# Optimization experiments

Measured on AMD Instinct MI355X. Metric: run time of the kernel, lower is better.

The kernel has to match this reference:

```python
import jax, jax.numpy as jnp
import numpy as np

TOPK = 2
ALPHA = 32.0
EPS = 1e-20


def setup_inputs() -> dict:
    key = jax.random.key(0)
    ks = jax.random.split(key, 6)
    E, D, R, Q, V = 16, 2048, 16, 2048, 512
    B, S = 2, 2048
    return {
        "hidden_states": jax.random.normal(ks[0], (B, S, D), jnp.float32),
        "router_weight": jax.random.normal(ks[1], (E, D), jnp.float32) * 0.02,
        "q_lora_a": jax.random.normal(ks[2], (E, D, R), jnp.float32) * 0.02,
        "q_lora_b": jax.random.normal(ks[3], (E, R, Q), jnp.float32) * 0.02,
        "v_lora_a": jax.random.normal(ks[4], (E, D, R), jnp.float32) * 0.02,
        "v_lora_b": jax.random.normal(ks[5], (E, R, V), jnp.float32) * 0.02,
    }


def reference(hidden_states, router_weight, q_lora_a, q_lora_b, v_lora_a, v_lora_b):
    E, D, R = q_lora_a.shape
    Qo = q_lora_b.shape[-1]
    Vo = v_lora_b.shape[-1]
    scale = ALPHA / float(R)
    orig_shape = hidden_states.shape[:-1]
    h = hidden_states.reshape(-1, D)  # [n, D]
    n = h.shape[0]

    # router: top-k softmax probs, renormalized over the k selected experts
    logits = jnp.einsum('nd,ed->ne', h, router_weight)
    probs = jax.nn.softmax(logits, axis=-1)
    scores, idx = jax.lax.top_k(probs, TOPK)          # [n, k]
    scores = scores / (scores.sum(-1, keepdims=True) + EPS)

    # per-token expert combine weights c[n, e] = scale * sum_k score_k * 1[idx_k == e]
    c = jnp.zeros((n, E), h.dtype).at[jnp.arange(n)[:, None], idx].add(scores * scale)

    # dense per-expert low-rank projections; weighting by c makes non-selected
    # experts contribute zero -> identical math to gather + einsum + weighted sum.
    q_low = jnp.einsum('nd,edr->ner', h, q_lora_a) * c[..., None]  # [n, E, R]
    v_low = jnp.einsum('nd,edr->ner', h, v_lora_a) * c[..., None]
    q_delta = jnp.einsum('ner,erq->nq', q_low, q_lora_b)
    v_delta = jnp.einsum('ner,erv->nv', v_low, v_lora_b)

    return (q_delta.reshape(*orig_shape, Qo), v_delta.reshape(*orig_shape, Vo))
```

## Files before the change

kernel.cpp:

```cpp
#include <hip/hip_runtime.h>
#include <math.h>

#define DD 2048
#define EE 16
#define RR 16
#define QO 2048
#define VO 512
#define TILE 128
#define BATCH 16
#define DSPLIT 4
#define DRANGE (DD / DSPLIT)
#define DC 64
#define HSTR (DC + 4)
#define ASTR 20
#define RDC 256
#define T2 32
#define CGQ (QO / 256)
#define CGV (VO / 256)

struct Route { int i0, i1; float w0, w1; };

__global__ __launch_bounds__(256) void router_kernel(
    const float* __restrict__ h, const float* __restrict__ rw,
    Route* __restrict__ route, int n)
{
    __shared__ float  hs[8 * RDC];
    __shared__ double slogd[8 * EE];

    int t0 = blockIdx.x * 8;
    int e  = threadIdx.x >> 4;
    int l  = threadIdx.x & 15;

    double acc[8];
#pragma unroll
    for (int t = 0; t < 8; ++t) acc[t] = 0.0;

    for (int d0 = 0; d0 < DD; d0 += RDC) {
        __syncthreads();
        for (int i = threadIdx.x; i < 8 * (RDC / 4); i += 256) {
            int t = i >> 6, dq = (i & 63) * 4;
            float4 v = make_float4(0.f, 0.f, 0.f, 0.f);
            if (t0 + t < n)
                v = *(const float4*)&h[(size_t)(t0 + t) * DD + d0 + dq];
            *(float4*)&hs[t * RDC + dq] = v;
        }
        __syncthreads();
        const float* rwe = rw + e * DD + d0;
#pragma unroll
        for (int g = 0; g < RDC / 64; ++g) {
            int d = g * 64 + l * 4;
            float4 r4 = *(const float4*)&rwe[d];
            double rx = r4.x, ry = r4.y, rz = r4.z, rw4 = r4.w;
#pragma unroll
            for (int t = 0; t < 8; ++t) {
                float4 hv = *(const float4*)&hs[t * RDC + d];
                acc[t] += (double)hv.x * rx + (double)hv.y * ry
                        + (double)hv.z * rz + (double)hv.w * rw4;
            }
        }
    }
#pragma unroll
    for (int t = 0; t < 8; ++t) {
#pragma unroll
        for (int off = 8; off; off >>= 1)
            acc[t] += __shfl_down(acc[t], off, 16);
    }
    if (l == 0) {
#pragma unroll
        for (int t = 0; t < 8; ++t) slogd[t * EE + e] = acc[t];
    }
    __syncthreads();

    if (threadIdx.x < 8) {
        int t = threadIdx.x, tok = t0 + t;
        if (tok < n) {
            double lg[EE];
#pragma unroll
            for (int i = 0; i < EE; ++i) lg[i] = slogd[t * EE + i];
            int i0 = 0;
            for (int i = 1; i < EE; ++i) if (lg[i] > lg[i0]) i0 = i;
            int i1 = -1;
            for (int i = 0; i < EE; ++i)
                if (i != i0 && (i1 < 0 || lg[i] > lg[i1])) i1 = i;
            double mx = lg[i0], Z = 0.0;
            for (int i = 0; i < EE; ++i) Z += exp(lg[i] - mx);
            double p0 = 1.0 / Z;
            double p1 = exp(lg[i1] - mx) / Z;
            double s  = p0 + p1 + 1e-20;
            Route rt;
            rt.i0 = i0; rt.i1 = i1;
            rt.w0 = (float)(2.0 * p0 / s);
            rt.w1 = (float)(2.0 * p1 / s);
            route[tok] = rt;
        }
    }
}

__global__ __launch_bounds__(256) void a_kernel(
    const float* __restrict__ h, const Route* __restrict__ route,
    const float* __restrict__ qa, const float* __restrict__ va,
    float* __restrict__ low, int n)
{
    int e  = blockIdx.x;
    int t0 = blockIdx.y * TILE;
    int ds = blockIdx.z;

    __shared__ int   sel_tok[TILE];
    __shared__ float sel_w[TILE];
    __shared__ int   sel_k[TILE];
    __shared__ int   sm_cnt;
    if (threadIdx.x == 0) sm_cnt = 0;
    __syncthreads();
    for (int i = threadIdx.x; i < TILE; i += 256) {
        int tok = t0 + i;
        if (tok < n) {
            Route rt = route[tok];
            float w = 0.f; int sel = 0, k = 0;
            if      (rt.i0 == e) { sel = 1; w = rt.w0; k = 0; }
            else if (rt.i1 == e) { sel = 1; w = rt.w1; k = 1; }
            if (sel) {
                int p = atomicAdd(&sm_cnt, 1);
                sel_tok[p] = tok; sel_w[p] = w; sel_k[p] = k;
            }
        }
    }
    __syncthreads();
    int m = sm_cnt;
    if (m == 0) return;

    __align__(16) __shared__ float aq_s[DC * ASTR];
    __align__(16) __shared__ float av_s[DC * ASTR];
    __align__(16) __shared__ float hs[BATCH * HSTR];

    const float* qa_e = qa + (size_t)e * DD * RR;
    const float* va_e = va + (size_t)e * DD * RR;

    int s    = threadIdx.x & 15;
    int tile = threadIdx.x >> 4;
    int tp   = tile >> 2;
    int rp   = tile & 3;

    for (int b0 = 0; b0 < m; b0 += BATCH) {
        int mb = min(BATCH, m - b0);

        float accq[4][4], accv[4][4];
#pragma unroll
        for (int ti = 0; ti < 4; ++ti)
#pragma unroll
            for (int ri = 0; ri < 4; ++ri) { accq[ti][ri] = 0.f; accv[ti][ri] = 0.f; }

        for (int d0 = ds * DRANGE; d0 < (ds + 1) * DRANGE; d0 += DC) {
            __syncthreads();
            {
                int i = threadIdx.x;
                int d = i >> 2, rf = (i & 3) * 4;
                *(float4*)&aq_s[d * ASTR + rf] = *(const float4*)&qa_e[(size_t)(d0 + d) * RR + rf];
                *(float4*)&av_s[d * ASTR + rf] = *(const float4*)&va_e[(size_t)(d0 + d) * RR + rf];
            }
            {
                int i = threadIdx.x;
                int j = i >> 4, dq = (i & 15) * 4;
                float4 v = make_float4(0.f, 0.f, 0.f, 0.f);
                if (j < mb)
                    v = *(const float4*)&h[(size_t)sel_tok[b0 + j] * DD + d0 + dq];
                *(float4*)&hs[j * HSTR + dq] = v;
            }
            __syncthreads();
#pragma unroll
            for (int dd = 0; dd < DC / 16; ++dd) {
                int d = (dd << 4) + s;
                float hv[4];
#pragma unroll
                for (int ti = 0; ti < 4; ++ti)
                    hv[ti] = hs[(tp * 4 + ti) * HSTR + d];
                float4 aqv = *(const float4*)&aq_s[d * ASTR + rp * 4];
                float4 avv = *(const float4*)&av_s[d * ASTR + rp * 4];
                const float* aqp = &aqv.x;
                const float* avp = &avv.x;
#pragma unroll
                for (int ti = 0; ti < 4; ++ti)
#pragma unroll
                    for (int ri = 0; ri < 4; ++ri) {
                        accq[ti][ri] = fmaf(hv[ti], aqp[ri], accq[ti][ri]);
                        accv[ti][ri] = fmaf(hv[ti], avp[ri], accv[ti][ri]);
                    }
            }
        }
#pragma unroll
        for (int ti = 0; ti < 4; ++ti)
#pragma unroll
            for (int ri = 0; ri < 4; ++ri) {
#pragma unroll
                for (int off = 8; off; off >>= 1) {
                    accq[ti][ri] += __shfl_down(accq[ti][ri], off, 16);
                    accv[ti][ri] += __shfl_down(accv[ti][ri], off, 16);
                }
            }
        if (s == 0) {
#pragma unroll
            for (int ti = 0; ti < 4; ++ti) {
                int t = tp * 4 + ti;
                if (t < mb) {
                    int   tok = sel_tok[b0 + t];
                    int   k   = sel_k[b0 + t];
                    float w   = sel_w[b0 + t];
                    size_t base = ((size_t)(tok * 2 + k) * DSPLIT + ds) * 32;
#pragma unroll
                    for (int ri = 0; ri < 4; ++ri) {
                        low[base + rp * 4 + ri]      = accq[ti][ri] * w;
                        low[base + 16 + rp * 4 + ri] = accv[ti][ri] * w;
                    }
                }
            }
        }
        __syncthreads();
    }
}

__global__ __launch_bounds__(256) void b_kernel(
    const Route* __restrict__ route, const float* __restrict__ low,
    const float* __restrict__ qb, const float* __restrict__ vb,
    float* __restrict__ outq, float* __restrict__ outv, int n)
{
    int t0 = blockIdx.x * T2;
    int cg = blockIdx.y;
    int tid = threadIdx.x;

    __shared__ float acc_s[T2 * 256];
    __shared__ float ls[T2 * 2 * RR];
    __shared__ int   elist[EE * T2];
    __shared__ int   ecnt[EE];
    __shared__ Route rts[T2];

    if (tid < EE) ecnt[tid] = 0;
    if (tid < T2) {
        int tok = t0 + tid;
        if (tok < n) rts[tid] = route[tok];
        else { rts[tid].i0 = -1; rts[tid].i1 = -1; rts[tid].w0 = 0.f; rts[tid].w1 = 0.f; }
    }
    __syncthreads();
    if (tid < T2 * 2) {
        int j = tid >> 1, k = tid & 1;
        int e = k ? rts[j].i1 : rts[j].i0;
        if (e >= 0) {
            int p = atomicAdd(&ecnt[e], 1);
            elist[e * T2 + p] = j * 2 + k;
        }
    }
    int side = (cg >= CGQ) ? 1 : 0;
    {
        int slot = tid >> 2, r4 = (tid & 3) * 4;
        int j = slot >> 1, k = slot & 1;
        int tok = t0 + j;
        float4 v = make_float4(0.f, 0.f, 0.f, 0.f);
        if (tok < n) {
            const float* lp = low + (size_t)(tok * 2 + k) * (DSPLIT * 32) + side * 16 + r4;
            float4 p0 = *(const float4*)(lp);
            float4 p1 = *(const float4*)(lp + 32);
            float4 p2 = *(const float4*)(lp + 64);
            float4 p3 = *(const float4*)(lp + 96);
            v.x = p0.x + p1.x + p2.x + p3.x;
            v.y = p0.y + p1.y + p2.y + p3.y;
            v.z = p0.z + p1.z + p2.z + p3.z;
            v.w = p0.w + p1.w + p2.w + p3.w;
        }
        *(float4*)&ls[slot * RR + r4] = v;
    }
#pragma unroll
    for (int j = 0; j < T2; ++j) acc_s[j * 256 + tid] = 0.f;
    __syncthreads();

    const float* bp; float* outp; int W, colbase;
    if (cg < CGQ) { bp = qb; outp = outq; W = QO; colbase = cg * 256; }
    else          { bp = vb; outp = outv; W = VO; colbase = (cg - CGQ) * 256; }
    int col = colbase + tid;

    for (int e = 0; e < EE; ++e) {
        int c = ecnt[e];
        if (c == 0) continue;
        const float* be = bp + (size_t)e * RR * W + col;
        float bc[RR];
#pragma unroll
        for (int r = 0; r < RR; ++r) bc[r] = be[(size_t)r * W];
        for (int ii = 0; ii < c; ++ii) {
            int sk = elist[e * T2 + ii];
            int j  = sk >> 1;
            const float* lp = &ls[sk * RR];
            float4 l0 = *(const float4*)(lp);
            float4 l1 = *(const float4*)(lp + 4);
            float4 l2 = *(const float4*)(lp + 8);
            float4 l3 = *(const float4*)(lp + 12);
            float v = 0.f;
            v = fmaf(l0.x, bc[0],  v); v = fmaf(l0.y, bc[1],  v);
            v = fmaf(l0.z, bc[2],  v); v = fmaf(l0.w, bc[3],  v);
            v = fmaf(l1.x, bc[4],  v); v = fmaf(l1.y, bc[5],  v);
            v = fmaf(l1.z, bc[6],  v); v = fmaf(l1.w, bc[7],  v);
            v = fmaf(l2.x, bc[8],  v); v = fmaf(l2.y, bc[9],  v);
            v = fmaf(l2.z, bc[10], v); v = fmaf(l2.w, bc[11], v);
            v = fmaf(l3.x, bc[12], v); v = fmaf(l3.y, bc[13], v);
            v = fmaf(l3.z, bc[14], v); v = fmaf(l3.w, bc[15], v);
            acc_s[j * 256 + tid] += v;
        }
    }
#pragma unroll
    for (int j = 0; j < T2; ++j) {
        int tok = t0 + j;
        if (tok < n) outp[(size_t)tok * W + col] = acc_s[j * 256 + tid];
    }
}

extern "C" void kernel_launch(void* const* d_in, const int* in_sizes, int n_in,
                              void* d_out, int out_size, void* d_ws, size_t ws_size,
                              hipStream_t stream) {
    const float* h  = (const float*)d_in[0];
    const float* rw = (const float*)d_in[1];
    const float* qa = (const float*)d_in[2];
    const float* qb = (const float*)d_in[3];
    const float* va = (const float*)d_in[4];
    const float* vb = (const float*)d_in[5];

    int n = in_sizes[0] / DD;
    float* out  = (float*)d_out;
    float* outq = out;
    float* outv = out + (size_t)n * QO;

    Route* route = (Route*)d_ws;
    float* low   = (float*)((char*)d_ws + (((size_t)n * 16 + 255) & ~(size_t)255));

    int tiles = (n + TILE - 1) / TILE;

    router_kernel<<<(n + 7) / 8, 256, 0, stream>>>(h, rw, route, n);

    dim3 g2(EE, tiles, DSPLIT);
    a_kernel<<<g2, 256, 0, stream>>>(h, route, qa, va, low, n);

    dim3 g3((n + T2 - 1) / T2, CGQ + CGV);
    b_kernel<<<g3, 256, 0, stream>>>(route, low, qb, vb, outq, outv, n);
}
```

Measured before the change: 222.2 us.

## Bucket tokens per expert in router and compact A-kernel work over buckets

The router now appends each token-slot to a per-expert bucket through global atomics, so the A kernel walks dense per-expert lists in chunks of 32 tokens. Before, it scanned 128-token tiles and compacted locally, which left many blocks with sparse or empty work. Each thread now holds 8 tokens instead of 4, stores use float4, and the B kernel double-buffers expert B-weight loads into registers while writing per-slot partials instead of accumulating. The softmax weight math is also reduced to a closed form using only the top-two logits. The costs are an extra zero-count launch, contention on global atomics, the ushort token encoding (n*2 must fit in 16 bits), and a nondeterministic bucket order.

```diff
diff --git a/kernel.cpp b/kernel.cpp
--- a/kernel.cpp
+++ b/kernel.cpp
@@ -6,23 +6,28 @@
 #define RR 16
 #define QO 2048
 #define VO 512
-#define TILE 128
-#define BATCH 16
 #define DSPLIT 4
 #define DRANGE (DD / DSPLIT)
 #define DC 64
 #define HSTR (DC + 4)
 #define ASTR 20
 #define RDC 256
+#define TB 32
+#define ACHUNKS 32
 #define T2 32
 #define CGQ (QO / 256)
 #define CGV (VO / 256)
 
 struct Route { int i0, i1; float w0, w1; };
 
+__global__ void zero_cnt(int* __restrict__ cnt) {
+    if (threadIdx.x < EE) cnt[threadIdx.x] = 0;
+}
+
 __global__ __launch_bounds__(256) void router_kernel(
     const float* __restrict__ h, const float* __restrict__ rw,
-    Route* __restrict__ route, int n)
+    Route* __restrict__ route, unsigned short* __restrict__ bucket,
+    int* __restrict__ cnt, int n)
 {
     __shared__ float  hs[8 * RDC];
     __shared__ double slogd[8 * EE];
@@ -82,55 +87,37 @@
             int i1 = -1;
             for (int i = 0; i < EE; ++i)
                 if (i != i0 && (i1 < 0 || lg[i] > lg[i1])) i1 = i;
-            double mx = lg[i0], Z = 0.0;
-            for (int i = 0; i < EE; ++i) Z += exp(lg[i] - mx);
-            double p0 = 1.0 / Z;
-            double p1 = exp(lg[i1] - mx) / Z;
-            double s  = p0 + p1 + 1e-20;
+            double ed = exp(lg[i1] - lg[i0]);
+            double w0 = 2.0 / (1.0 + ed);
             Route rt;
             rt.i0 = i0; rt.i1 = i1;
-            rt.w0 = (float)(2.0 * p0 / s);
-            rt.w1 = (float)(2.0 * p1 / s);
+            rt.w0 = (float)w0;
+            rt.w1 = (float)(2.0 - w0);
             route[tok] = rt;
+            int p0 = atomicAdd(&cnt[i0], 1);
+            bucket[(size_t)i0 * n + p0] = (unsigned short)(tok * 2);
+            int p1 = atomicAdd(&cnt[i1], 1);
+            bucket[(size_t)i1 * n + p1] = (unsigned short)(tok * 2 + 1);
         }
     }
 }
 
 __global__ __launch_bounds__(256) void a_kernel(
     const float* __restrict__ h, const Route* __restrict__ route,
+    const unsigned short* __restrict__ bucket, const int* __restrict__ cnt,
     const float* __restrict__ qa, const float* __restrict__ va,
     float* __restrict__ low, int n)
 {
     int e  = blockIdx.x;
-    int t0 = blockIdx.y * TILE;
     int ds = blockIdx.z;
-
-    __shared__ int   sel_tok[TILE];
-    __shared__ float sel_w[TILE];
-    __shared__ int   sel_k[TILE];
-    __shared__ int   sm_cnt;
-    if (threadIdx.x == 0) sm_cnt = 0;
-    __syncthreads();
-    for (int i = threadIdx.x; i < TILE; i += 256) {
-        int tok = t0 + i;
-        if (tok < n) {
-            Route rt = route[tok];
-            float w = 0.f; int sel = 0, k = 0;
-            if      (rt.i0 == e) { sel = 1; w = rt.w0; k = 0; }
-            else if (rt.i1 == e) { sel = 1; w = rt.w1; k = 1; }
-            if (sel) {
-                int p = atomicAdd(&sm_cnt, 1);
-                sel_tok[p] = tok; sel_w[p] = w; sel_k[p] = k;
-            }
-        }
-    }
-    __syncthreads();
-    int m = sm_cnt;
-    if (m == 0) return;
-
+    int cnt_e = cnt[e];
+
+    __shared__ int   sel_tok[TB];
+    __shared__ int   sel_k[TB];
+    __shared__ float sel_w[TB];
     __align__(16) __shared__ float aq_s[DC * ASTR];
     __align__(16) __shared__ float av_s[DC * ASTR];
-    __align__(16) __shared__ float hs[BATCH * HSTR];
+    __align__(16) __shared__ float hs[TB * HSTR];
 
     const float* qa_e = qa + (size_t)e * DD * RR;
     const float* va_e = va + (size_t)e * DD * RR;
@@ -140,12 +127,19 @@
     int tp   = tile >> 2;
     int rp   = tile & 3;
 
-    for (int b0 = 0; b0 < m; b0 += BATCH) {
-        int mb = min(BATCH, m - b0);
-
-        float accq[4][4], accv[4][4];
-#pragma unroll
-        for (int ti = 0; ti < 4; ++ti)
+    for (int c0 = blockIdx.y * TB; c0 < cnt_e; c0 += gridDim.y * TB) {
+        int mb = min(TB, cnt_e - c0);
+        if (threadIdx.x < TB && threadIdx.x < mb) {
+            int slot = bucket[(size_t)e * n + c0 + threadIdx.x];
+            int tok = slot >> 1, k = slot & 1;
+            Route rt = route[tok];
+            sel_tok[threadIdx.x] = tok;
+            sel_k[threadIdx.x]   = k;
+            sel_w[threadIdx.x]   = k ? rt.w1 : rt.w0;
+        }
+        float accq[8][4], accv[8][4];
+#pragma unroll
+        for (int ti = 0; ti < 8; ++ti)
 #pragma unroll
             for (int ri = 0; ri < 4; ++ri) { accq[ti][ri] = 0.f; accv[ti][ri] = 0.f; }
 
@@ -157,28 +151,27 @@
                 *(float4*)&aq_s[d * ASTR + rf] = *(const float4*)&qa_e[(size_t)(d0 + d) * RR + rf];
                 *(float4*)&av_s[d * ASTR + rf] = *(const float4*)&va_e[(size_t)(d0 + d) * RR + rf];
             }
-            {
-                int i = threadIdx.x;
+            for (int i = threadIdx.x; i < TB * (DC / 4); i += 256) {
                 int j = i >> 4, dq = (i & 15) * 4;
                 float4 v = make_float4(0.f, 0.f, 0.f, 0.f);
                 if (j < mb)
-                    v = *(const float4*)&h[(size_t)sel_tok[b0 + j] * DD + d0 + dq];
+                    v = *(const float4*)&h[(size_t)sel_tok[j] * DD + d0 + dq];
                 *(float4*)&hs[j * HSTR + dq] = v;
             }
             __syncthreads();
 #pragma unroll
             for (int dd = 0; dd < DC / 16; ++dd) {
                 int d = (dd << 4) + s;
-                float hv[4];
-#pragma unroll
-                for (int ti = 0; ti < 4; ++ti)
-                    hv[ti] = hs[(tp * 4 + ti) * HSTR + d];
+                float hv[8];
+#pragma unroll
+                for (int ti = 0; ti < 8; ++ti)
+                    hv[ti] = hs[(tp * 8 + ti) * HSTR + d];
                 float4 aqv = *(const float4*)&aq_s[d * ASTR + rp * 4];
                 float4 avv = *(const float4*)&av_s[d * ASTR + rp * 4];
                 const float* aqp = &aqv.x;
                 const float* avp = &avv.x;
 #pragma unroll
-                for (int ti = 0; ti < 4; ++ti)
+                for (int ti = 0; ti < 8; ++ti)
 #pragma unroll
                     for (int ri = 0; ri < 4; ++ri) {
                         accq[ti][ri] = fmaf(hv[ti], aqp[ri], accq[ti][ri]);
@@ -187,7 +180,7 @@
             }
         }
 #pragma unroll
-        for (int ti = 0; ti < 4; ++ti)
+        for (int ti = 0; ti < 8; ++ti)
 #pragma unroll
             for (int ri = 0; ri < 4; ++ri) {
 #pragma unroll
@@ -198,18 +191,19 @@
             }
         if (s == 0) {
 #pragma unroll
-            for (int ti = 0; ti < 4; ++ti) {
-                int t = tp * 4 + ti;
+            for (int ti = 0; ti < 8; ++ti) {
+                int t = tp * 8 + ti;
                 if (t < mb) {
-                    int   tok = sel_tok[b0 + t];
-                    int   k   = sel_k[b0 + t];
-                    float w   = sel_w[b0 + t];
+                    int   tok = sel_tok[t];
+                    int   k   = sel_k[t];
+                    float w   = sel_w[t];
                     size_t base = ((size_t)(tok * 2 + k) * DSPLIT + ds) * 32;
-#pragma unroll
-                    for (int ri = 0; ri < 4; ++ri) {
-                        low[base + rp * 4 + ri]      = accq[ti][ri] * w;
-                        low[base + 16 + rp * 4 + ri] = accv[ti][ri] * w;
-                    }
+                    float4 q4 = make_float4(accq[ti][0] * w, accq[ti][1] * w,
+                                            accq[ti][2] * w, accq[ti][3] * w);
+                    float4 v4 = make_float4(accv[ti][0] * w, accv[ti][1] * w,
+                                            accv[ti][2] * w, accv[ti][3] * w);
+                    *(float4*)&low[base + rp * 4]      = q4;
+                    *(float4*)&low[base + 16 + rp * 4] = v4;
                 }
             }
         }
@@ -226,7 +220,7 @@
     int cg = blockIdx.y;
     int tid = threadIdx.x;
 
-    __shared__ float acc_s[T2 * 256];
+    __shared__ float part[T2 * 2 * 256];
     __shared__ float ls[T2 * 2 * RR];
     __shared__ int   elist[EE * T2];
     __shared__ int   ecnt[EE];
@@ -266,8 +260,6 @@
         }
         *(float4*)&ls[slot * RR + r4] = v;
     }
-#pragma unroll
-    for (int j = 0; j < T2; ++j) acc_s[j * 256 + tid] = 0.f;
     __syncthreads();
 
     const float* bp; float* outp; int W, colbase;
@@ -275,37 +267,58 @@
     else          { bp = vb; outp = outv; W = VO; colbase = (cg - CGQ) * 256; }
     int col = colbase + tid;
 
-    for (int e = 0; e < EE; ++e) {
-        int c = ecnt[e];
-        if (c == 0) continue;
-        const float* be = bp + (size_t)e * RR * W + col;
-        float bc[RR];
-#pragma unroll
-        for (int r = 0; r < RR; ++r) bc[r] = be[(size_t)r * W];
-        for (int ii = 0; ii < c; ++ii) {
-            int sk = elist[e * T2 + ii];
-            int j  = sk >> 1;
-            const float* lp = &ls[sk * RR];
-            float4 l0 = *(const float4*)(lp);
-            float4 l1 = *(const float4*)(lp + 4);
-            float4 l2 = *(const float4*)(lp + 8);
-            float4 l3 = *(const float4*)(lp + 12);
-            float v = 0.f;
-            v = fmaf(l0.x, bc[0],  v); v = fmaf(l0.y, bc[1],  v);
-            v = fmaf(l0.z, bc[2],  v); v = fmaf(l0.w, bc[3],  v);
-            v = fmaf(l1.x, bc[4],  v); v = fmaf(l1.y, bc[5],  v);
-            v = fmaf(l1.z, bc[6],  v); v = fmaf(l1.w, bc[7],  v);
-            v = fmaf(l2.x, bc[8],  v); v = fmaf(l2.y, bc[9],  v);
-            v = fmaf(l2.z, bc[10], v); v = fmaf(l2.w, bc[11], v);
-            v = fmaf(l3.x, bc[12], v); v = fmaf(l3.y, bc[13], v);
-            v = fmaf(l3.z, bc[14], v); v = fmaf(l3.w, bc[15], v);
-            acc_s[j * 256 + tid] += v;
-        }
-    }
+    float bcA[RR], bcB[RR];
+    {
+        const float* be = bp + col;
+#pragma unroll
+        for (int r = 0; r < RR; ++r) bcA[r] = be[(size_t)r * W];
+    }
+
+#define PROC_E(EI, BC)                                                      \
+    {                                                                       \
+        int c = ecnt[EI];                                                   \
+        for (int ii = 0; ii < c; ++ii) {                                    \
+            int sk = elist[(EI) * T2 + ii];                                 \
+            const float* lp = &ls[sk * RR];                                 \
+            float4 l0 = *(const float4*)(lp);                               \
+            float4 l1 = *(const float4*)(lp + 4);                           \
+            float4 l2 = *(const float4*)(lp + 8);                           \
+            float4 l3 = *(const float4*)(lp + 12);                          \
+            float v = 0.f;                                                  \
+            v = fmaf(l0.x, BC[0],  v); v = fmaf(l0.y, BC[1],  v);           \
+            v = fmaf(l0.z, BC[2],  v); v = fmaf(l0.w, BC[3],  v);           \
+            v = fmaf(l1.x, BC[4],  v); v = fmaf(l1.y, BC[5],  v);           \
+            v = fmaf(l1.z, BC[6],  v); v = fmaf(l1.w, BC[7],  v);           \
+            v = fmaf(l2.x, BC[8],  v); v = fmaf(l2.y, BC[9],  v);           \
+            v = fmaf(l2.z, BC[10], v); v = fmaf(l2.w, BC[11], v);           \
+            v = fmaf(l3.x, BC[12], v); v = fmaf(l3.y, BC[13], v);           \
+            v = fmaf(l3.z, BC[14], v); v = fmaf(l3.w, BC[15], v);           \
+            part[sk * 256 + tid] = v;                                       \
+        }                                                                   \
+    }
+
+    for (int e = 0; e < EE; e += 2) {
+        {
+            const float* bn = bp + (size_t)(e + 1) * RR * W + col;
+#pragma unroll
+            for (int r = 0; r < RR; ++r) bcB[r] = bn[(size_t)r * W];
+        }
+        PROC_E(e, bcA);
+        if (e + 2 < EE) {
+            const float* bn = bp + (size_t)(e + 2) * RR * W + col;
+#pragma unroll
+            for (int r = 0; r < RR; ++r) bcA[r] = bn[(size_t)r * W];
+        }
+        PROC_E(e + 1, bcB);
+    }
+#undef PROC_E
+
 #pragma unroll
     for (int j = 0; j < T2; ++j) {
         int tok = t0 + j;
-        if (tok < n) outp[(size_t)tok * W + col] = acc_s[j * 256 + tid];
+        if (tok < n)
+            outp[(size_t)tok * W + col] =
+                part[(j * 2) * 256 + tid] + part[(j * 2 + 1) * 256 + tid];
     }
 }
 
@@ -324,15 +337,21 @@
     float* outq = out;
     float* outv = out + (size_t)n * QO;
 
-    Route* route = (Route*)d_ws;
-    float* low   = (float*)((char*)d_ws + (((size_t)n * 16 + 255) & ~(size_t)255));
-
-    int tiles = (n + TILE - 1) / TILE;
-
-    router_kernel<<<(n + 7) / 8, 256, 0, stream>>>(h, rw, route, n);
-
-    dim3 g2(EE, tiles, DSPLIT);
-    a_kernel<<<g2, 256, 0, stream>>>(h, route, qa, va, low, n);
+    char* ws = (char*)d_ws;
+    Route* route = (Route*)ws;
+    size_t off = ((size_t)n * sizeof(Route) + 255) & ~(size_t)255;
+    int* cnt = (int*)(ws + off);
+    off = (off + EE * sizeof(int) + 255) & ~(size_t)255;
+    unsigned short* bucket = (unsigned short*)(ws + off);
+    off = (off + (size_t)EE * n * sizeof(unsigned short) + 255) & ~(size_t)255;
+    float* low = (float*)(ws + off);
+
+    zero_cnt<<<1, 64, 0, stream>>>(cnt);
+
+    router_kernel<<<(n + 7) / 8, 256, 0, stream>>>(h, rw, route, bucket, cnt, n);
+
+    dim3 g2(EE, ACHUNKS, DSPLIT);
+    a_kernel<<<g2, 256, 0, stream>>>(h, route, bucket, cnt, qa, va, low, n);
 
     dim3 g3((n + T2 - 1) / T2, CGQ + CGV);
     b_kernel<<<g3, 256, 0, stream>>>(route, low, qb, vb, outq, outv, n);
```

After: 243.0 us. 9.4% more time.
